# Kernel optimization log

Measured on AMD Instinct MI355X. Metric: run time of the kernel, lower is better.

The kernel has to match this reference:

```python
import jax, jax.numpy as jnp
import numpy as np
import math

L = 6        # num_layers
H = 16       # nhead
D = 1024     # feature_dim (= d_model, dim_factor=1)
DFF = 1024
IN = 1024    # input_dim
B, T = 16, 512
HD = D // H
EPS = 1e-5


def _get_slopes(n):
    def pow2(n):
        start = 2.0 ** (-2.0 ** (-(math.log2(n) - 3)))
        return [start * (start ** i) for i in range(n)]
    if math.log2(n).is_integer():
        return pow2(n)
    cp2 = 2 ** math.floor(math.log2(n))
    return pow2(cp2) + _get_slopes(2 * cp2)[0::2][: n - cp2]


def _alibi_bias(num_heads, seq_len):
    # init_alibi_biased_mask_future reduces to -slope_h * |i - j|
    slopes = jnp.asarray(_get_slopes(num_heads), dtype=jnp.float32)  # [H]
    idx = jnp.arange(seq_len)
    rel = -jnp.abs(idx[:, None] - idx[None, :]).astype(jnp.float32)  # [T,T]
    return slopes[:, None, None] * rel  # [H,T,T]


def _ln(x, w, b):
    m = jnp.mean(x, axis=-1, keepdims=True)
    v = jnp.mean(jnp.square(x - m), axis=-1, keepdims=True)
    return (x - m) * jax.lax.rsqrt(v + EPS) * w + b


def setup_inputs() -> dict:
    key = jax.random.key(0)
    ks = jax.random.split(key, 16)
    s = 0.02
    return {
        "x": jax.random.normal(ks[0], (B, T, IN), dtype=jnp.float32),
        "bn_w": jax.random.normal(ks[1], (D, IN), dtype=jnp.float32) * s,
        "bn_b": jnp.zeros((D,), jnp.float32),
        "qkv_w": jax.random.normal(ks[2], (L, 3 * D, D), dtype=jnp.float32) * s,
        "qkv_b": jnp.zeros((L, 3 * D), jnp.float32),
        "out_w": jax.random.normal(ks[3], (L, D, D), dtype=jnp.float32) * s,
        "out_b": jnp.zeros((L, D), jnp.float32),
        "ln1_w": jnp.ones((L, D), jnp.float32),
        "ln1_b": jnp.zeros((L, D), jnp.float32),
        "ln2_w": jnp.ones((L, D), jnp.float32),
        "ln2_b": jnp.zeros((L, D), jnp.float32),
        "ff1_w": jax.random.normal(ks[4], (L, DFF, D), dtype=jnp.float32) * s,
        "ff1_b": jnp.zeros((L, DFF), jnp.float32),
        "ff2_w": jax.random.normal(ks[5], (L, D, DFF), dtype=jnp.float32) * s,
        "ff2_b": jnp.zeros((L, D), jnp.float32),
    }


def reference(x, bn_w, bn_b, qkv_w, qkv_b, out_w, out_b,
              ln1_w, ln1_b, ln2_w, ln2_b, ff1_w, ff1_b, ff2_w, ff2_b):
    b, t, _ = x.shape
    bias = _alibi_bias(H, t)  # [H,T,T], same for all batch elements
    h = x @ bn_w.T + bn_b  # bottleneck -> [B,T,D]
    scale = 1.0 / math.sqrt(HD)
    for l in range(L):
        qkv = h @ qkv_w[l].T + qkv_b[l]  # [B,T,3D]
        q, k, v = jnp.split(qkv, 3, axis=-1)
        q = q.reshape(b, t, H, HD)
        k = k.reshape(b, t, H, HD)
        v = v.reshape(b, t, H, HD)
        scores = jnp.einsum('bihd,bjhd->bhij', q, k) * scale + bias[None]
        attn = jax.nn.softmax(scores, axis=-1)
        o = jnp.einsum('bhij,bjhd->bihd', attn, v).reshape(b, t, D)
        o = o @ out_w[l].T + out_b[l]
        h = _ln(h + o, ln1_w[l], ln1_b[l])  # post-norm (PyTorch default)
        f = jax.nn.gelu(h @ ff1_w[l].T + ff1_b[l], approximate=False)
        f = f @ ff2_w[l].T + ff2_b[l]
        h = _ln(h + f, ln2_w[l], ln2_b[l])
    return h
```

## Files before the change

kernel.cpp:

```cpp
#include <hip/hip_runtime.h>
#include <stdint.h>

#define DEV static __device__ __forceinline__

typedef __attribute__((ext_vector_type(8))) uint16_t u16x8;
typedef __attribute__((ext_vector_type(4))) uint16_t u16x4;
typedef __attribute__((ext_vector_type(4))) uint32_t u32x4;
typedef __attribute__((ext_vector_type(4))) float    f32x4;
typedef __attribute__((ext_vector_type(8))) __bf16   bf16x8;

typedef __attribute__((address_space(3))) void lds_void;
typedef __attribute__((address_space(1))) void gbl_void;

DEV float bf2f(uint16_t u){
  union { uint32_t i; float f; } v; v.i = ((uint32_t)u) << 16; return v.f;
}
DEV uint16_t f2bf(float f){ return __builtin_bit_cast(uint16_t, (__bf16)f); }
DEV f32x4 mfma16(u16x8 a, u16x8 b, f32x4 c){
  return __builtin_amdgcn_mfma_f32_16x16x32_bf16(
      __builtin_bit_cast(bf16x8, a), __builtin_bit_cast(bf16x8, b), c, 0, 0, 0);
}
DEV uint32_t cvt_pk_bf16(float lo, float hi){
  uint32_t r;
  asm("v_cvt_pk_bf16_f32 %0, %1, %2" : "=v"(r) : "v"(lo), "v"(hi));
  return r;
}

__global__ __launch_bounds__(256)
void te_cvt(const float* __restrict__ in, uint16_t* __restrict__ out)
{
  const size_t i = ((size_t)blockIdx.x * 256 + threadIdx.x) * 8;
  f32x4 a = *(const f32x4*)(in + i);
  f32x4 b = *(const f32x4*)(in + i + 4);
  u16x8 o;
#pragma unroll
  for (int e = 0; e < 4; e++) {
    o[e]     = f2bf(a[e]);
    o[e + 4] = f2bf(b[e]);
  }
  *(u16x8*)(out + i) = o;
}

template<int MODE>
__global__ __launch_bounds__(256)
void te_gemm_bb(const uint16_t* __restrict__ A, int lda,
                const uint16_t* __restrict__ W, const float* __restrict__ bias,
                uint16_t* __restrict__ outB, int M, int N, int K)
{
  __shared__ uint16_t la[128 * 64];
  __shared__ uint16_t lb[128 * 64];
  const int tid = threadIdx.x;
  const int w = tid >> 6, l = tid & 63;
  const int lr = l & 15, lg = l >> 4;
  const int tm = blockIdx.y * 128, tn = blockIdx.x * 128;
  const int srow = l >> 3;
  const int scol = ((l & 7) ^ srow) * 8;
  const int wr = (w >> 1) * 64, wc = (w & 1) * 64;

  f32x4 acc[4][4] = {};

  for (int k0 = 0; k0 < K; k0 += 64) {
#pragma unroll
    for (int c = 0; c < 4; c++) {
      const int rb = (c * 4 + w) * 8;
      const uint16_t* ga = A + (size_t)(tm + rb + srow) * lda + (k0 + scol);
      __builtin_amdgcn_global_load_lds((gbl_void*)(uintptr_t)ga,
                                       (lds_void*)(la + rb * 64), 16, 0, 0);
      const uint16_t* gw = W + (size_t)(tn + rb + srow) * K + (k0 + scol);
      __builtin_amdgcn_global_load_lds((gbl_void*)(uintptr_t)gw,
                                       (lds_void*)(lb + rb * 64), 16, 0, 0);
    }
    __syncthreads();
#pragma unroll
    for (int kk = 0; kk < 2; kk++) {
      u16x8 af[4], bfr[4];
#pragma unroll
      for (int i = 0; i < 4; i++) {
        const int row = wr + i * 16 + lr;
        af[i] = *(const u16x8*)&la[row * 64 + (((kk * 4 + lg) ^ (lr & 7)) << 3)];
      }
#pragma unroll
      for (int j = 0; j < 4; j++) {
        const int row = wc + j * 16 + lr;
        bfr[j] = *(const u16x8*)&lb[row * 64 + (((kk * 4 + lg) ^ (lr & 7)) << 3)];
      }
      __builtin_amdgcn_s_setprio(1);
#pragma unroll
      for (int i = 0; i < 4; i++)
#pragma unroll
        for (int j = 0; j < 4; j++)
          acc[i][j] = mfma16(af[i], bfr[j], acc[i][j]);
      __builtin_amdgcn_s_setprio(0);
    }
    __syncthreads();
  }

  float bv[4];
#pragma unroll
  for (int j = 0; j < 4; j++) bv[j] = bias[tn + wc + j * 16 + lr];
#pragma unroll
  for (int i = 0; i < 4; i++)
#pragma unroll
    for (int j = 0; j < 4; j++)
#pragma unroll
      for (int r = 0; r < 4; r++) {
        const int row = tm + wr + i * 16 + lg * 4 + r;
        const int col = tn + wc + j * 16 + lr;
        float v = acc[i][j][r] + bv[j];
        if (MODE == 2) {
          const float u = 0.7978845608028654f * v * (1.0f + 0.044715f * v * v);
          const float t = 1.0f - 2.0f / (__expf(2.0f * u) + 1.0f);
          v = 0.5f * v * (1.0f + t);
        }
        outB[(size_t)row * N + col] = f2bf(v);
      }
}

#define SOFTMAX_PACK(S, MR, SDQ, ACC, IQ, P2)                                  \
  {                                                                            \
    const float f0 = (float)((IQ) - jt - lg * 4);                              \
    float mt = -1e30f;                                                         \
    _Pragma("unroll")                                                          \
    for (int n = 0; n < 4; n++) {                                              \
      const float fj = f0 - (float)(n * 16);                                   \
      _Pragma("unroll")                                                        \
      for (int r = 0; r < 4; r++) {                                            \
        const float v = fmaf(S[n][r], scl2e, -slope2e * fabsf(fj - (float)r)); \
        S[n][r] = v;                                                           \
        mt = fmaxf(mt, v);                                                     \
      }                                                                        \
    }                                                                          \
    mt = fmaxf(mt, __shfl_xor(mt, 16));                                        \
    mt = fmaxf(mt, __shfl_xor(mt, 32));                                        \
    if (!__all(mt <= MR)) {                                                    \
      const float mN = fmaxf(MR, mt);                                          \
      const float fq = exp2f(MR - mN);                                         \
      MR = mN;                                                                 \
      SDQ *= fq;                                                               \
      float fA[4];                                                             \
      _Pragma("unroll")                                                        \
      for (int r = 0; r < 4; r++) fA[r] = __shfl(fq, lg * 4 + r);              \
      _Pragma("unroll")                                                        \
      for (int n = 0; n < 4; n++)                                              \
        _Pragma("unroll")                                                      \
        for (int r = 0; r < 4; r++) ACC[n][r] *= fA[r];                        \
    }                                                                          \
    float rs = 0.0f;                                                           \
    _Pragma("unroll")                                                          \
    for (int n = 0; n < 4; n++)                                                \
      _Pragma("unroll")                                                        \
      for (int r = 0; r < 4; r++) {                                            \
        const float p = exp2f(S[n][r] - MR);                                   \
        S[n][r] = p;                                                           \
        rs += p;                                                               \
      }                                                                        \
    rs += __shfl_xor(rs, 16);                                                  \
    rs += __shfl_xor(rs, 32);                                                  \
    SDQ += rs;                                                                 \
    _Pragma("unroll")                                                          \
    for (int n = 0; n < 4; n++) {                                              \
      P2[n][0] = cvt_pk_bf16(S[n][0], S[n][1]);                                \
      P2[n][1] = cvt_pk_bf16(S[n][2], S[n][3]);                                \
    }                                                                          \
  }

__global__ __launch_bounds__(256)
void te_attn(uint16_t* __restrict__ qkv)
{
  __shared__ uint16_t kl[64 * 64];
  __shared__ uint16_t vt[64 * 64];
  const int tid = threadIdx.x;
  const int w = tid >> 6, l = tid & 63;
  const int lr = l & 15, lg = l >> 4;
  const int bh = blockIdx.x, qt = blockIdx.y;
  const int h = bh & 15, b = bh >> 4;

  const int iQ0 = qt * 128 + w * 16 + lr;
  u16x8 qf[2][2];
#pragma unroll
  for (int g = 0; g < 2; g++) {
    const size_t qoff = ((size_t)(b * 512 + iQ0 + g * 64)) * 3072 + h * 64 + lg * 8;
    qf[g][0] = *(const u16x8*)&qkv[qoff];
    qf[g][1] = *(const u16x8*)&qkv[qoff + 32];
  }
  const float LOG2E = 1.4426950408889634f;
  const float scl2e = 0.125f * LOG2E;
  const float slope2e = exp2f(-0.5f * (float)(h + 1)) * LOG2E;

  const int sjb = tid >> 3;
  const int sd0 = (tid & 7) * 8;

  float mR0 = -1e30f, sdq0 = 0.0f, mR1 = -1e30f, sdq1 = 0.0f;
  f32x4 acc0[4] = {}, acc1[4] = {};

  u16x8 kreg[2], vreg[2];
  {
    const int jt0 = (qt * 2) * 64;
#pragma unroll
    for (int cc = 0; cc < 2; cc++) {
      const int j = sjb + cc * 32;
      const size_t rbase = ((size_t)(b * 512 + jt0 + j)) * 3072 + h * 64 + sd0;
      kreg[cc] = *(const u16x8*)&qkv[rbase + 1024];
      vreg[cc] = *(const u16x8*)&qkv[rbase + 2048];
    }
  }

  for (int step = 0; step < 8; step++) {
    const int jt = ((qt * 2 + step) & 7) * 64;
#pragma unroll
    for (int cc = 0; cc < 2; cc++) {
      const int j = sjb + cc * 32;
      *(u16x8*)&kl[j * 64 + (((sd0 >> 3) ^ (j & 7)) << 3)] = kreg[cc];
      const int cV = (((j >> 3) ^ (sd0 >> 3)) << 3) + (j & 7);
#pragma unroll
      for (int e = 0; e < 8; e++) vt[(sd0 + e) * 64 + cV] = vreg[cc][e];
    }
    __syncthreads();
    if (step < 7) {
      const int jtn = ((qt * 2 + step + 1) & 7) * 64;
#pragma unroll
      for (int cc = 0; cc < 2; cc++) {
        const int j = sjb + cc * 32;
        const size_t rbase = ((size_t)(b * 512 + jtn + j)) * 3072 + h * 64 + sd0;
        kreg[cc] = *(const u16x8*)&qkv[rbase + 1024];
        vreg[cc] = *(const u16x8*)&qkv[rbase + 2048];
      }
    }

    f32x4 s0[4] = {}, s1[4] = {};
#pragma unroll
    for (int kk = 0; kk < 2; kk++) {
      u16x8 kf[4];
#pragma unroll
      for (int n = 0; n < 4; n++) {
        const int row = n * 16 + lr;
        kf[n] = *(const u16x8*)&kl[row * 64 + (((kk * 4 + lg) ^ (lr & 7)) << 3)];
      }
      __builtin_amdgcn_s_setprio(1);
#pragma unroll
      for (int n = 0; n < 4; n++) {
        s0[n] = mfma16(kf[n], qf[0][kk], s0[n]);
        s1[n] = mfma16(kf[n], qf[1][kk], s1[n]);
      }
      __builtin_amdgcn_s_setprio(0);
    }

    uint32_t P2a[4][2], P2b[4][2];
    SOFTMAX_PACK(s0, mR0, sdq0, acc0, iQ0,      P2a);
    SOFTMAX_PACK(s1, mR1, sdq1, acc1, iQ0 + 64, P2b);

#pragma unroll
    for (int kk = 0; kk < 2; kk++) {
      uint32_t pw0[4], pw1[4];
#pragma unroll
      for (int t = 0; t < 4; t++) {
        const int srcLane = lr + 16 * ((lg & 1) * 2 + (t >> 1));
        const uint32_t a0 = __shfl(P2a[2 * kk + 0][t & 1], srcLane);
        const uint32_t b0 = __shfl(P2a[2 * kk + 1][t & 1], srcLane);
        pw0[t] = (lg >> 1) ? b0 : a0;
        const uint32_t a1 = __shfl(P2b[2 * kk + 0][t & 1], srcLane);
        const uint32_t b1 = __shfl(P2b[2 * kk + 1][t & 1], srcLane);
        pw1[t] = (lg >> 1) ? b1 : a1;
      }
      u32x4 q0 = { pw0[0], pw0[1], pw0[2], pw0[3] };
      u32x4 q1 = { pw1[0], pw1[1], pw1[2], pw1[3] };
      u16x8 pf0 = __builtin_bit_cast(u16x8, q0);
      u16x8 pf1 = __builtin_bit_cast(u16x8, q1);
      u16x8 vf[4];
#pragma unroll
      for (int n = 0; n < 4; n++) {
        const int row = n * 16 + lr;
        vf[n] = *(const u16x8*)&vt[row * 64 + ((((kk * 4 + lg) ^ (2 * n + (lr >> 3))) & 7) << 3)];
      }
      __builtin_amdgcn_s_setprio(1);
#pragma unroll
      for (int n = 0; n < 4; n++) {
        acc0[n] = mfma16(pf0, vf[n], acc0[n]);
        acc1[n] = mfma16(pf1, vf[n], acc1[n]);
      }
      __builtin_amdgcn_s_setprio(0);
    }
    __syncthreads();
  }

  {
    float sdA[4];
#pragma unroll
    for (int r = 0; r < 4; r++) sdA[r] = 1.0f / __shfl(sdq0, lg * 4 + r);
#pragma unroll
    for (int n = 0; n < 4; n++)
#pragma unroll
      for (int r = 0; r < 4; r++) {
        const int i = qt * 128 + w * 16 + lg * 4 + r;
        const int d = h * 64 + n * 16 + lr;
        qkv[((size_t)(b * 512 + i)) * 3072 + d] = f2bf(acc0[n][r] * sdA[r]);
      }
  }
  {
    float sdA[4];
#pragma unroll
    for (int r = 0; r < 4; r++) sdA[r] = 1.0f / __shfl(sdq1, lg * 4 + r);
#pragma unroll
    for (int n = 0; n < 4; n++)
#pragma unroll
      for (int r = 0; r < 4; r++) {
        const int i = qt * 128 + 64 + w * 16 + lg * 4 + r;
        const int d = h * 64 + n * 16 + lr;
        qkv[((size_t)(b * 512 + i)) * 3072 + d] = f2bf(acc1[n][r] * sdA[r]);
      }
  }
}

template<int FINAL>
__global__ __launch_bounds__(256)
void te_ln(const uint16_t* __restrict__ h, const uint16_t* __restrict__ delta,
           const float* __restrict__ w, const float* __restrict__ b,
           uint16_t* __restrict__ hout, float* __restrict__ fout)
{
  const int row = blockIdx.x, t = threadIdx.x;
  const size_t base = (size_t)row * 1024 + t * 4;
  u16x4 hv = *(const u16x4*)&h[base];
  u16x4 dv = *(const u16x4*)&delta[base];
  float x[4];
#pragma unroll
  for (int i = 0; i < 4; i++) x[i] = bf2f(hv[i]) + bf2f(dv[i]);
  float s = x[0] + x[1] + x[2] + x[3];
  float ss = x[0]*x[0] + x[1]*x[1] + x[2]*x[2] + x[3]*x[3];
#pragma unroll
  for (int msk = 32; msk >= 1; msk >>= 1) {
    s  += __shfl_xor(s, msk);
    ss += __shfl_xor(ss, msk);
  }
  __shared__ float rs[4], rq[4];
  const int wv = t >> 6;
  if ((t & 63) == 0) { rs[wv] = s; rq[wv] = ss; }
  __syncthreads();
  s  = rs[0] + rs[1] + rs[2] + rs[3];
  ss = rq[0] + rq[1] + rq[2] + rq[3];
  const float mean = s * (1.0f / 1024.0f);
  const float var  = ss * (1.0f / 1024.0f) - mean * mean;
  const float rstd = rsqrtf(var + 1e-5f);
  f32x4 wv4 = *(const f32x4*)&w[t * 4];
  f32x4 bv4 = *(const f32x4*)&b[t * 4];
  if (FINAL == 0) {
    u16x4 bo;
#pragma unroll
    for (int i = 0; i < 4; i++)
      bo[i] = f2bf((x[i] - mean) * rstd * wv4[i] + bv4[i]);
    *(u16x4*)&hout[base] = bo;
  } else {
    f32x4 yo;
#pragma unroll
    for (int i = 0; i < 4; i++)
      yo[i] = (x[i] - mean) * rstd * wv4[i] + bv4[i];
    *(f32x4*)&fout[base] = yo;
  }
}

extern "C" void kernel_launch(void* const* d_in, const int* in_sizes, int n_in,
                              void* d_out, int out_size, void* d_ws, size_t ws_size,
                              hipStream_t stream)
{
  (void)in_sizes; (void)n_in; (void)out_size; (void)ws_size;
  const float* x     = (const float*)d_in[0];
  const float* bn_w  = (const float*)d_in[1];
  const float* bn_b  = (const float*)d_in[2];
  const float* qkv_w = (const float*)d_in[3];
  const float* qkv_b = (const float*)d_in[4];
  const float* out_w = (const float*)d_in[5];
  const float* out_b = (const float*)d_in[6];
  const float* ln1_w = (const float*)d_in[7];
  const float* ln1_b = (const float*)d_in[8];
  const float* ln2_w = (const float*)d_in[9];
  const float* ln2_b = (const float*)d_in[10];
  const float* ff1_w = (const float*)d_in[11];
  const float* ff1_b = (const float*)d_in[12];
  const float* ff2_w = (const float*)d_in[13];
  const float* ff2_b = (const float*)d_in[14];

  char* ws = (char*)d_ws;
  uint16_t* h_bf    = (uint16_t*)ws;
  uint16_t* qkvb    = (uint16_t*)(ws + (16u  << 20));
  uint16_t* scrA    = (uint16_t*)(ws + (64u  << 20));
  uint16_t* qkvw_bf = (uint16_t*)(ws + (80u  << 20));
  uint16_t* ff2w_bf = (uint16_t*)(ws + (116u << 20));
  uint16_t* bnw_bf  = (uint16_t*)(ws + (128u << 20));
  uint16_t* outw_bf = (uint16_t*)d_out;
  uint16_t* ff1w_bf = (uint16_t*)((char*)d_out + (12u << 20));
  float*    outf    = (float*)d_out;

  const int M = 8192;
  dim3 blk(256);

  te_cvt<<<dim3(18874368 / 2048), blk, 0, stream>>>(qkv_w, qkvw_bf);
  te_cvt<<<dim3(6291456  / 2048), blk, 0, stream>>>(out_w, outw_bf);
  te_cvt<<<dim3(6291456  / 2048), blk, 0, stream>>>(ff1_w, ff1w_bf);
  te_cvt<<<dim3(6291456  / 2048), blk, 0, stream>>>(ff2_w, ff2w_bf);
  te_cvt<<<dim3(1048576  / 2048), blk, 0, stream>>>(bn_w,  bnw_bf);
  te_cvt<<<dim3(8388608  / 2048), blk, 0, stream>>>(x,     scrA);

  te_gemm_bb<0><<<dim3(8, 64), blk, 0, stream>>>(scrA, 1024, bnw_bf, bn_b,
                                                 h_bf, M, 1024, 1024);

  for (int l = 0; l < 6; l++) {
    te_gemm_bb<0><<<dim3(24, 64), blk, 0, stream>>>(
        h_bf, 1024, qkvw_bf + (size_t)l * 3072 * 1024, qkv_b + l * 3072,
        qkvb, M, 3072, 1024);
    te_attn<<<dim3(256, 4), blk, 0, stream>>>(qkvb);
    te_gemm_bb<0><<<dim3(8, 64), blk, 0, stream>>>(
        qkvb, 3072, outw_bf + (size_t)l * 1024 * 1024, out_b + l * 1024,
        scrA, M, 1024, 1024);
    te_ln<0><<<dim3(8192), blk, 0, stream>>>(h_bf, scrA, ln1_w + l * 1024, ln1_b + l * 1024,
                                             h_bf, nullptr);
    te_gemm_bb<2><<<dim3(8, 64), blk, 0, stream>>>(
        h_bf, 1024, ff1w_bf + (size_t)l * 1024 * 1024, ff1_b + l * 1024,
        scrA, M, 1024, 1024);
    te_gemm_bb<0><<<dim3(8, 64), blk, 0, stream>>>(
        scrA, 1024, ff2w_bf + (size_t)l * 1024 * 1024, ff2_b + l * 1024,
        qkvb, M, 1024, 1024);
    if (l == 5) {
      te_ln<1><<<dim3(8192), blk, 0, stream>>>(h_bf, qkvb, ln2_w + l * 1024, ln2_b + l * 1024,
                                               nullptr, outf);
    } else {
      te_ln<0><<<dim3(8192), blk, 0, stream>>>(h_bf, qkvb, ln2_w + l * 1024, ln2_b + l * 1024,
                                               h_bf, nullptr);
    }
  }
}
```

Measured before the change: 1.474 ms.

## Replace GEMM with double-buffered 256x128 tile kernel using 512 threads

Rewrites the bf16 MFMA GEMM to use 256x128 output tiles computed by 8 waves of 512 threads. Global-to-LDS loads are double-buffered so the next K-tile streams in while the current one computes, with a vmcnt wait replacing the full syncthreads. Blocks are launched on a 1D grid with an XCD-aware remap that groups neighbouring tiles for L2 locality. It uses more LDS (96KB) and lowers occupancy, and adds extra barriers per K-step.

```diff
diff --git a/kernel.cpp b/kernel.cpp
--- a/kernel.cpp
+++ b/kernel.cpp
@@ -42,71 +42,112 @@
 }
 
 template<int MODE>
-__global__ __launch_bounds__(256)
-void te_gemm_bb(const uint16_t* __restrict__ A, int lda,
-                const uint16_t* __restrict__ W, const float* __restrict__ bias,
-                uint16_t* __restrict__ outB, int M, int N, int K)
+__global__ __launch_bounds__(512)
+void te_gemm256(const uint16_t* __restrict__ A, int lda,
+                const uint16_t* __restrict__ Wm, const float* __restrict__ bias,
+                uint16_t* __restrict__ outB, int N, int K)
 {
-  __shared__ uint16_t la[128 * 64];
-  __shared__ uint16_t lb[128 * 64];
+  constexpr int SZA = 256 * 64;
+  constexpr int SZB = 128 * 64;
+  __shared__ uint16_t lds[2 * (SZA + SZB)];
+
   const int tid = threadIdx.x;
   const int w = tid >> 6, l = tid & 63;
   const int lr = l & 15, lg = l >> 4;
-  const int tm = blockIdx.y * 128, tn = blockIdx.x * 128;
-  const int srow = l >> 3;
-  const int scol = ((l & 7) ^ srow) * 8;
-  const int wr = (w >> 1) * 64, wc = (w & 1) * 64;
-
-  f32x4 acc[4][4] = {};
-
-  for (int k0 = 0; k0 < K; k0 += 64) {
+  const int wr = w >> 2, wc = w & 3;
+  const int srow = l >> 3, chunk = l & 7;
+
+  const int nb = gridDim.x;
+  const int bid = blockIdx.x;
+  const int lid = (bid & 7) * (nb >> 3) + (bid >> 3);
+  const int nx = N >> 7;
+  const int tm = (lid / nx) << 8;
+  const int tn = (lid % nx) << 7;
+
+  const int rw = w * 8 + srow;
+  const int sc = (chunk ^ srow) << 3;
+
+  auto stage = [&](int kt, int p) {
+    const int k0 = kt << 6;
+    uint16_t* bufA = lds + p * (SZA + SZB);
+    uint16_t* bufB = bufA + SZA;
 #pragma unroll
     for (int c = 0; c < 4; c++) {
-      const int rb = (c * 4 + w) * 8;
-      const uint16_t* ga = A + (size_t)(tm + rb + srow) * lda + (k0 + scol);
+      const uint16_t* ga = A + (size_t)(tm + c * 64 + rw) * lda + (k0 + sc);
       __builtin_amdgcn_global_load_lds((gbl_void*)(uintptr_t)ga,
-                                       (lds_void*)(la + rb * 64), 16, 0, 0);
-      const uint16_t* gw = W + (size_t)(tn + rb + srow) * K + (k0 + scol);
+          (lds_void*)(bufA + (c * 64 + w * 8) * 64), 16, 0, 0);
+    }
+#pragma unroll
+    for (int c = 0; c < 2; c++) {
+      const uint16_t* gw = Wm + (size_t)(tn + c * 64 + rw) * K + (k0 + sc);
       __builtin_amdgcn_global_load_lds((gbl_void*)(uintptr_t)gw,
-                                       (lds_void*)(lb + rb * 64), 16, 0, 0);
-    }
-    __syncthreads();
-#pragma unroll
-    for (int kk = 0; kk < 2; kk++) {
-      u16x8 af[4], bfr[4];
-#pragma unroll
-      for (int i = 0; i < 4; i++) {
-        const int row = wr + i * 16 + lr;
-        af[i] = *(const u16x8*)&la[row * 64 + (((kk * 4 + lg) ^ (lr & 7)) << 3)];
-      }
-#pragma unroll
-      for (int j = 0; j < 4; j++) {
-        const int row = wc + j * 16 + lr;
-        bfr[j] = *(const u16x8*)&lb[row * 64 + (((kk * 4 + lg) ^ (lr & 7)) << 3)];
-      }
+          (lds_void*)(bufB + (c * 64 + w * 8) * 64), 16, 0, 0);
+    }
+  };
+
+  f32x4 acc[8][2] = {};
+  const int nt = K >> 6;
+
+  stage(0, 0);
+  for (int t = 0; t < nt; ++t) {
+    const int cur = t & 1;
+    uint16_t* bufA = lds + cur * (SZA + SZB);
+    uint16_t* bufB = bufA + SZA;
+
+    asm volatile("" ::: "memory");
+    if (t + 1 < nt) {
+      stage(t + 1, cur ^ 1);
+      asm volatile("s_waitcnt vmcnt(6)" ::: "memory");
+    } else {
+      asm volatile("s_waitcnt vmcnt(0)" ::: "memory");
+    }
+    __builtin_amdgcn_s_barrier();
+
+    u16x8 bf[2][2];
+#pragma unroll
+    for (int fc = 0; fc < 2; fc++)
+#pragma unroll
+      for (int kk = 0; kk < 2; kk++) {
+        const int nrow = wc * 32 + fc * 16 + lr;
+        bf[fc][kk] = *(const u16x8*)&bufB[nrow * 64 + (((kk * 4 + lg) ^ (lr & 7)) << 3)];
+      }
+
+#pragma unroll
+    for (int q = 0; q < 4; q++) {
+      u16x8 af[2][2];
+#pragma unroll
+      for (int i = 0; i < 2; i++)
+#pragma unroll
+        for (int kk = 0; kk < 2; kk++) {
+          const int row = wr * 128 + (q * 2 + i) * 16 + lr;
+          af[i][kk] = *(const u16x8*)&bufA[row * 64 + (((kk * 4 + lg) ^ (lr & 7)) << 3)];
+        }
+      __builtin_amdgcn_s_barrier();
       __builtin_amdgcn_s_setprio(1);
 #pragma unroll
-      for (int i = 0; i < 4; i++)
-#pragma unroll
-        for (int j = 0; j < 4; j++)
-          acc[i][j] = mfma16(af[i], bfr[j], acc[i][j]);
+      for (int i = 0; i < 2; i++)
+#pragma unroll
+        for (int fc = 0; fc < 2; fc++) {
+          acc[q * 2 + i][fc] = mfma16(af[i][0], bf[fc][0], acc[q * 2 + i][fc]);
+          acc[q * 2 + i][fc] = mfma16(af[i][1], bf[fc][1], acc[q * 2 + i][fc]);
+        }
       __builtin_amdgcn_s_setprio(0);
-    }
-    __syncthreads();
-  }
-
-  float bv[4];
-#pragma unroll
-  for (int j = 0; j < 4; j++) bv[j] = bias[tn + wc + j * 16 + lr];
-#pragma unroll
-  for (int i = 0; i < 4; i++)
-#pragma unroll
-    for (int j = 0; j < 4; j++)
+      __builtin_amdgcn_s_barrier();
+    }
+  }
+
+  float bv[2];
+#pragma unroll
+  for (int fc = 0; fc < 2; fc++) bv[fc] = bias[tn + wc * 32 + fc * 16 + lr];
+#pragma unroll
+  for (int fr = 0; fr < 8; fr++)
+#pragma unroll
+    for (int fc = 0; fc < 2; fc++)
 #pragma unroll
       for (int r = 0; r < 4; r++) {
-        const int row = tm + wr + i * 16 + lg * 4 + r;
-        const int col = tn + wc + j * 16 + lr;
-        float v = acc[i][j][r] + bv[j];
+        const int row = tm + wr * 128 + fr * 16 + lg * 4 + r;
+        const int col = tn + wc * 32 + fc * 16 + lr;
+        float v = acc[fr][fc][r] + bv[fc];
         if (MODE == 2) {
           const float u = 0.7978845608028654f * v * (1.0f + 0.044715f * v * v);
           const float t = 1.0f - 2.0f / (__expf(2.0f * u) + 1.0f);
@@ -389,8 +430,8 @@
   uint16_t* ff1w_bf = (uint16_t*)((char*)d_out + (12u << 20));
   float*    outf    = (float*)d_out;
 
-  const int M = 8192;
   dim3 blk(256);
+  dim3 blk512(512);
 
   te_cvt<<<dim3(18874368 / 2048), blk, 0, stream>>>(qkv_w, qkvw_bf);
   te_cvt<<<dim3(6291456  / 2048), blk, 0, stream>>>(out_w, outw_bf);
@@ -399,25 +440,25 @@
   te_cvt<<<dim3(1048576  / 2048), blk, 0, stream>>>(bn_w,  bnw_bf);
   te_cvt<<<dim3(8388608  / 2048), blk, 0, stream>>>(x,     scrA);
 
-  te_gemm_bb<0><<<dim3(8, 64), blk, 0, stream>>>(scrA, 1024, bnw_bf, bn_b,
-                                                 h_bf, M, 1024, 1024);
+  te_gemm256<0><<<dim3(256), blk512, 0, stream>>>(scrA, 1024, bnw_bf, bn_b,
+                                                  h_bf, 1024, 1024);
 
   for (int l = 0; l < 6; l++) {
-    te_gemm_bb<0><<<dim3(24, 64), blk, 0, stream>>>(
+    te_gemm256<0><<<dim3(768), blk512, 0, stream>>>(
         h_bf, 1024, qkvw_bf + (size_t)l * 3072 * 1024, qkv_b + l * 3072,
-        qkvb, M, 3072, 1024);
+        qkvb, 3072, 1024);
     te_attn<<<dim3(256, 4), blk, 0, stream>>>(qkvb);
-    te_gemm_bb<0><<<dim3(8, 64), blk, 0, stream>>>(
+    te_gemm256<0><<<dim3(256), blk512, 0, stream>>>(
         qkvb, 3072, outw_bf + (size_t)l * 1024 * 1024, out_b + l * 1024,
-        scrA, M, 1024, 1024);
+        scrA, 1024, 1024);
     te_ln<0><<<dim3(8192), blk, 0, stream>>>(h_bf, scrA, ln1_w + l * 1024, ln1_b + l * 1024,
                                              h_bf, nullptr);
-    te_gemm_bb<2><<<dim3(8, 64), blk, 0, stream>>>(
+    te_gemm256<2><<<dim3(256), blk512, 0, stream>>>(
         h_bf, 1024, ff1w_bf + (size_t)l * 1024 * 1024, ff1_b + l * 1024,
-        scrA, M, 1024, 1024);
-    te_gemm_bb<0><<<dim3(8, 64), blk, 0, stream>>>(
+        scrA, 1024, 1024);
+    te_gemm256<0><<<dim3(256), blk512, 0, stream>>>(
         scrA, 1024, ff2w_bf + (size_t)l * 1024 * 1024, ff2_b + l * 1024,
-        qkvb, M, 1024, 1024);
+        qkvb, 1024, 1024);
     if (l == 5) {
       te_ln<1><<<dim3(8192), blk, 0, stream>>>(h_bf, qkvb, ln2_w + l * 1024, ln2_b + l * 1024,
                                                nullptr, outf);
```

Result: faster. 1.404 ms (-4.8%).
